# Kernel optimization log

Hardware: AMD Instinct MI355X
Metric: run time of the kernel (lower is better)

Reference implementation:

```python
import jax, jax.numpy as jnp
import numpy as np
from jax import lax

PATCH = 32  # enc conv kernel/stride
EPS = 1e-12  # F.normalize eps


def setup_inputs() -> dict:
    key = jax.random.key(0)
    ks = jax.random.split(key, 7)
    B, N, H, W = 32, 256, 32, 32
    fdim, vdim = 512, 128
    x = jax.random.normal(ks[0], (B, 3 * N, H, W), dtype=jnp.float32)
    conv_w = jax.random.normal(ks[1], (fdim, 3, PATCH, PATCH), dtype=jnp.float32) * (1.0 / np.sqrt(3 * PATCH * PATCH))
    conv_b = jax.random.normal(ks[2], (fdim,), dtype=jnp.float32) * 0.01
    fc1_w = jax.random.normal(ks[3], (vdim, fdim), dtype=jnp.float32) * (1.0 / np.sqrt(fdim))
    fc1_b = jax.random.normal(ks[4], (vdim,), dtype=jnp.float32) * 0.01
    # deterministic dropout masks (p=0.5, train mode -> keep * 1/(1-p))
    drop1 = (jax.random.uniform(ks[5], (B, N, N)) >= 0.5).astype(jnp.float32) * 2.0
    drop2 = (jax.random.uniform(ks[6], (B, N, N)) >= 0.5).astype(jnp.float32) * 2.0
    return {"x": x, "conv_w": conv_w, "conv_b": conv_b,
            "fc1_w": fc1_w, "fc1_b": fc1_b, "drop1": drop1, "drop2": drop2}


def _branch(scores, drop, eye):
    # softmax over dim=-2, zero diag, dropout, L1-normalize over dim=-2
    P = jax.nn.softmax(scores, axis=-2)
    P = P * (1.0 - eye)
    P = P * drop
    denom = jnp.maximum(jnp.sum(jnp.abs(P), axis=-2, keepdims=True), EPS)
    return P / denom


def reference(x, conv_w, conv_b, fc1_w, fc1_b, drop1, drop2):
    B, C, H, W = x.shape
    N = C // 3
    xi = x.reshape(B * N, 3, H, W)
    # enc: patchify conv -> (B*N, fdim, 1, 1)
    fm = lax.conv_general_dilated(xi, conv_w, (PATCH, PATCH), 'VALID',
                                  dimension_numbers=('NCHW', 'OIHW', 'NCHW'))
    fm = fm + conv_b[None, :, None, None]
    # map2vec: adaptive avgpool(1,1) + flatten + fc1
    v = fm.mean(axis=(2, 3))                      # (B*N, fdim)
    v = v @ fc1_w.T + fc1_b                       # (B*N, vdim)
    f = v.reshape(B, N, -1)                       # (B, N, vdim)
    f_norm = f / jnp.maximum(jnp.linalg.norm(f, axis=-1, keepdims=True), EPS)
    A = jnp.einsum('bnd,bmd->bnm', f_norm, f_norm)  # cosine affinity (B,N,N)
    Atemp = A * (128.0 ** 0.5)                    # torch.div(A, 1/128**0.5)
    eye = jnp.eye(N, dtype=A.dtype)
    A1 = _branch(Atemp, drop1, eye)
    A2t = _branch(jnp.swapaxes(Atemp, -1, -2), drop2, eye)
    AtA = jnp.swapaxes(jnp.matmul(A2t, A1), -1, -2)
    # nll_loss(AtA, arange targets) == -mean of diagonal entries
    diag = jnp.einsum('bii->bi', AtA)
    loss = -jnp.mean(diag)
    return f, A, loss
```

## Files before the change

kernel.cpp:

```cpp
#include <hip/hip_runtime.h>
#include <stdint.h>

#define S_SCALE 11.313708498984761f
#define EPS 1e-12f

typedef __bf16 bf16x8 __attribute__((ext_vector_type(8)));
typedef float  f32x4  __attribute__((ext_vector_type(4)));

__device__ __forceinline__ f32x4 mfma16(bf16x8 a, bf16x8 b, f32x4 c) {
  return __builtin_amdgcn_mfma_f32_16x16x32_bf16(a, b, c, 0, 0, 0);
}

__device__ __forceinline__ float waveSum(float v) {
#pragma unroll
  for (int m = 32; m > 0; m >>= 1) v += __shfl_xor(v, m, 64);
  return v;
}

__device__ __forceinline__ void load_lds16(const float* g, float* l) {
  __builtin_amdgcn_global_load_lds(
      (const __attribute__((address_space(1))) uint32_t*)g,
      (__attribute__((address_space(3))) uint32_t*)l, 16, 0, 0);
}

#define OFF_W    0
#define OFF_BIAS 786432
#define OFF_FN   786944
#define OFF_ZP   2884096
#define OFF_P1   3146240

__global__ __launch_bounds__(256) void k_fusew2(const float* __restrict__ conv_w,
                                                const float* __restrict__ fc1_w,
                                                const float* __restrict__ conv_b,
                                                const float* __restrict__ fc1_b,
                                                __bf16* __restrict__ W,
                                                float* __restrict__ bias2,
                                                float* __restrict__ loss) {
  const int t = threadIdx.x;
  const int wave = t >> 6, lane = t & 63;
  if (blockIdx.x == 256) {
    if (t == 0) loss[0] = 0.f;
    for (int o = wave; o < 128; o += 4) {
      float p = 0.f;
#pragma unroll
      for (int c8 = 0; c8 < 8; ++c8)
        p = fmaf(fc1_w[o * 512 + c8 * 64 + lane], conv_b[c8 * 64 + lane], p);
      p = waveSum(p);
      if (lane == 0) bias2[o] = p + fc1_b[o];
    }
    return;
  }
  __shared__ float cw_s[64][12];
  __shared__ float fc1_s[128][65];
  const int k0 = blockIdx.x * 12;
  const int og = t >> 1, half = t & 1;
  const int kb = half * 6;
  float acc[6] = {};
  for (int cs = 0; cs < 8; ++cs) {
    const int cc = cs * 64;
    __syncthreads();
#pragma unroll
    for (int i = 0; i < 3; ++i) {
      int idx = t + 256 * i;
      int cr = idx / 12, kk = idx - cr * 12;
      cw_s[cr][kk] = conv_w[(cc + cr) * 3072 + k0 + kk];
    }
#pragma unroll
    for (int i = 0; i < 2; ++i) {
      int idx = t + 256 * i;
      int o = idx >> 2, c16 = (idx & 3) * 16;
#pragma unroll
      for (int q = 0; q < 4; ++q) {
        float4 v = *(const float4*)&fc1_w[o * 512 + cc + c16 + q * 4];
        fc1_s[o][c16 + q * 4 + 0] = v.x; fc1_s[o][c16 + q * 4 + 1] = v.y;
        fc1_s[o][c16 + q * 4 + 2] = v.z; fc1_s[o][c16 + q * 4 + 3] = v.w;
      }
    }
    __syncthreads();
    for (int ci = 0; ci < 64; ++ci) {
      float fv = fc1_s[og][ci];
#pragma unroll
      for (int j = 0; j < 6; ++j)
        acc[j] = fmaf(fv, cw_s[ci][kb + j], acc[j]);
    }
  }
#pragma unroll
  for (int j = 0; j < 6; ++j)
    W[og * 3072 + k0 + kb + j] = (__bf16)acc[j];
}


#define A_READS(BUF, AV)                                                      \
  _Pragma("unroll") for (int ks = 0; ks < 2; ++ks)                            \
      _Pragma("unroll") for (int mi = 0; mi < 2; ++mi) {                      \
    const int rb = (l15 + mi * 16) * 64;                                      \
    AV[ks][mi][0] =                                                           \
        *(const float4*)&A_lds[BUF][rb + (((ks * 8 + quad * 2) ^ l15) << 2)]; \
    AV[ks][mi][1] =                                                           \
        *(const float4*)&A_lds[BUF][rb + (((ks * 8 + quad * 2 + 1) ^ l15) << 2)]; \
  }

#define PREFETCH(IT, BUF, BB)                                                 \
  {                                                                           \
    const int kn = kbase + (IT) * 64;                                         \
    _Pragma("unroll") for (int j = 0; j < 2; ++j)                             \
        load_lds16(x + (m0 + dr[j]) * 3072 + kn + dc[j],                      \
                   &A_lds[BUF][(wave * 2 + j) * 256]);                        \
    _Pragma("unroll") for (int ks = 0; ks < 2; ++ks)                          \
        _Pragma("unroll") for (int ni = 0; ni < 2; ++ni)                      \
            BB[ks][ni] = *(const uint4*)(bp0 + ni * 49152 + (IT) * 64 + ks * 32); \
  }

#define COMPUTE(AV, BB)                                                       \
  _Pragma("unroll") for (int ks = 0; ks < 2; ++ks) {                          \
    bf16x8 afrag[2];                                                          \
    _Pragma("unroll") for (int mi = 0; mi < 2; ++mi) {                        \
      union { __bf16 h[8]; bf16x8 v; } pk;                                    \
      float4 lo = AV[ks][mi][0], hi = AV[ks][mi][1];                          \
      pk.h[0] = (__bf16)lo.x; pk.h[1] = (__bf16)lo.y;                         \
      pk.h[2] = (__bf16)lo.z; pk.h[3] = (__bf16)lo.w;                         \
      pk.h[4] = (__bf16)hi.x; pk.h[5] = (__bf16)hi.y;                         \
      pk.h[6] = (__bf16)hi.z; pk.h[7] = (__bf16)hi.w;                         \
      afrag[mi] = pk.v;                                                       \
    }                                                                         \
    _Pragma("unroll") for (int mi = 0; mi < 2; ++mi)                          \
        _Pragma("unroll") for (int ni = 0; ni < 2; ++ni)                      \
            acc[mi][ni] =                                                     \
        mfma16(afrag[mi], *(const bf16x8*)&BB[ks][ni], acc[mi][ni]);          \
  }

__global__ __launch_bounds__(256, 8) void k_gemm1(
    const float* __restrict__ x, const __bf16* __restrict__ W,
    float* __restrict__ P0, float* __restrict__ P1, float* __restrict__ P2,
    float* __restrict__ P3, float* __restrict__ P4, float* __restrict__ P5,
    float* __restrict__ P6, float* __restrict__ P7) {
  __shared__ __align__(16) float A_lds[2][32 * 64];
  const int t = threadIdx.x;
  const int wave = t >> 6, lane = t & 63;
  const int l15 = lane & 15, quad = lane >> 4;
  const int m0 = blockIdx.x * 32;
  const int kbase = blockIdx.y * 384;
  float* const Ps[8] = {P0, P1, P2, P3, P4, P5, P6, P7};
  float* P = Ps[blockIdx.y];

  int dr[2], dc[2];
#pragma unroll
  for (int j = 0; j < 2; ++j) {
    int row = wave * 8 + j * 4 + (lane >> 4);
    int cl = (lane & 15) ^ (row & 15);
    dr[j] = row;
    dc[j] = cl * 4;
  }
  const __bf16* bp0 = W + (wave * 32 + l15) * 3072 + quad * 8 + kbase;

  f32x4 acc[2][2] = {{{0.f,0.f,0.f,0.f},{0.f,0.f,0.f,0.f}},
                     {{0.f,0.f,0.f,0.f},{0.f,0.f,0.f,0.f}}};
  uint4 bA[2][2], bB[2][2];
  float4 av[2][2][2];

  PREFETCH(0, 0, bA)
  for (int it2 = 0; it2 < 3; ++it2) {
    const int it = it2 * 2;
    __syncthreads();
    A_READS(0, av)
    if (it + 1 < 6) PREFETCH(it + 1, 1, bB)
    COMPUTE(av, bA)
    __syncthreads();
    A_READS(1, av)
    if (it + 2 < 6) PREFETCH(it + 2, 0, bA)
    COMPUTE(av, bB)
  }
#pragma unroll
  for (int mi = 0; mi < 2; ++mi)
#pragma unroll
    for (int ni = 0; ni < 2; ++ni) {
      int col = wave * 32 + ni * 16 + l15;
#pragma unroll
      for (int r = 0; r < 4; ++r) {
        int row = m0 + mi * 16 + quad * 4 + r;
        P[row * 128 + col] = acc[mi][ni][r];
      }
    }
}

__global__ __launch_bounds__(256) void k_fin(
    float* __restrict__ f_inout, const float* __restrict__ P1,
    const float* __restrict__ P2, const float* __restrict__ P3,
    const float* __restrict__ P4, const float* __restrict__ P5,
    const float* __restrict__ P6, const float* __restrict__ P7,
    const float* __restrict__ bias2, __bf16* __restrict__ fn) {
  const int wave = threadIdx.x >> 6, lane = threadIdx.x & 63;
  const int row = blockIdx.x * 4 + wave;
  const int i0 = row * 128 + lane, i1 = i0 + 64;
  float v0 = f_inout[i0] + P1[i0] + P2[i0] + P3[i0] + P4[i0] + P5[i0] +
             P6[i0] + P7[i0] + bias2[lane];
  float v1 = f_inout[i1] + P1[i1] + P2[i1] + P3[i1] + P4[i1] + P5[i1] +
             P6[i1] + P7[i1] + bias2[lane + 64];
  float ss = waveSum(fmaf(v0, v0, v1 * v1));
  float inv = 1.f / fmaxf(sqrtf(ss), EPS);
  f_inout[i0] = v0;
  f_inout[i1] = v1;
  fn[i0] = (__bf16)(v0 * inv);
  fn[i1] = (__bf16)(v1 * inv);
}

__global__ __launch_bounds__(256) void k_gemm2(const __bf16* __restrict__ fn,
                                               const float* __restrict__ d1,
                                               const float* __restrict__ d2,
                                               float* __restrict__ Aout,
                                               float* __restrict__ Zp) {
  __shared__ __align__(16) __bf16 Li[64][136];
  __shared__ __align__(16) __bf16 Lj[64][136];
  __shared__ float zred[2][4][64];
  const int t = threadIdx.x;
  const int b = blockIdx.y;
  const int ti = blockIdx.x >> 2, tj = blockIdx.x & 3;
  const int i0 = ti * 64, j0 = tj * 64;
  const int wave = t >> 6, lane = t & 63;
  const int l15 = lane & 15, quad = lane >> 4;
  const __bf16* fb = fn + b * 32768;
#pragma unroll
  for (int i = 0; i < 4; ++i) {
    int idx = t + 256 * i;
    int r = idx >> 4, c8 = (idx & 15) * 8;
    *(uint4*)&Li[r][c8] = *(const uint4*)&fb[(i0 + r) * 128 + c8];
    *(uint4*)&Lj[r][c8] = *(const uint4*)&fb[(j0 + r) * 128 + c8];
  }
  __syncthreads();
  f32x4 acc[4] = {{0.f, 0.f, 0.f, 0.f}, {0.f, 0.f, 0.f, 0.f},
                  {0.f, 0.f, 0.f, 0.f}, {0.f, 0.f, 0.f, 0.f}};
#pragma unroll
  for (int ks = 0; ks < 4; ++ks) {
    bf16x8 af = *(const bf16x8*)&Li[wave * 16 + l15][ks * 32 + quad * 8];
#pragma unroll
    for (int nt = 0; nt < 4; ++nt) {
      bf16x8 bf = *(const bf16x8*)&Lj[nt * 16 + l15][ks * 32 + quad * 8];
      acc[nt] = mfma16(af, bf, acc[nt]);
    }
  }
  const int base = b * 65536;
  float* Ab = Aout + base;
  float z1c[4] = {0.f, 0.f, 0.f, 0.f}, z2c[4] = {0.f, 0.f, 0.f, 0.f};
#pragma unroll
  for (int nt = 0; nt < 4; ++nt) {
    int gj = j0 + nt * 16 + l15;
#pragma unroll
    for (int r = 0; r < 4; ++r) {
      int gi = i0 + wave * 16 + quad * 4 + r;
      float a = acc[nt][r];
      Ab[gi * 256 + gj] = a;
      float e = __expf(fmaf(S_SCALE, a, -S_SCALE));
      if (gi != gj) {
        int idx = base + gi * 256 + gj;
        z1c[nt] = fmaf(e, d1[idx], z1c[nt]);
        z2c[nt] = fmaf(e, d2[idx], z2c[nt]);
      }
    }
  }
#pragma unroll
  for (int nt = 0; nt < 4; ++nt) {
    z1c[nt] += __shfl_xor(z1c[nt], 16, 64);
    z1c[nt] += __shfl_xor(z1c[nt], 32, 64);
    z2c[nt] += __shfl_xor(z2c[nt], 16, 64);
    z2c[nt] += __shfl_xor(z2c[nt], 32, 64);
  }
  if (quad == 0) {
#pragma unroll
    for (int nt = 0; nt < 4; ++nt) {
      zred[0][wave][nt * 16 + l15] = z1c[nt];
      zred[1][wave][nt * 16 + l15] = z2c[nt];
    }
  }
  __syncthreads();
  if (t < 128) {
    int z = t >> 6, c = t & 63;
    float s = zred[z][0][c] + zred[z][1][c] + zred[z][2][c] + zred[z][3][c];
    Zp[(z * 4 + ti) * 8192 + b * 256 + j0 + c] = s;
  }
}

__global__ __launch_bounds__(256) void k_loss(const float* __restrict__ Aout,
                                              const float* __restrict__ d1,
                                              const float* __restrict__ d2,
                                              const float* __restrict__ Zp,
                                              float* __restrict__ loss) {
  __shared__ float d1s[64][65];
  __shared__ float z1s[64], z2s[64];
  __shared__ float red[4];
  const int t = threadIdx.x;
  const int b = blockIdx.y;
  const int ic = blockIdx.x >> 2, kc = blockIdx.x & 3;
  const int i0 = ic * 64, k0 = kc * 64;
  const int base = b * 65536;
  if (t < 64) {
    float s = 0.f;
#pragma unroll
    for (int p = 0; p < 4; ++p) s += Zp[p * 8192 + b * 256 + i0 + t];
    z1s[t] = 1.f / fmaxf(s, EPS);
  } else if (t < 128) {
    float s = 0.f;
#pragma unroll
    for (int p = 0; p < 4; ++p) s += Zp[(4 + p) * 8192 + b * 256 + k0 + t - 64];
    z2s[t - 64] = 1.f / fmaxf(s, EPS);
  }
#pragma unroll
  for (int ii = 0; ii < 16; ++ii) {
    int idx = t + 256 * ii;
    int kr = idx >> 6, ci = idx & 63;
    d1s[kr][ci] = d1[base + (k0 + kr) * 256 + i0 + ci];
  }
  __syncthreads();
  const int kl = t & 63, ig = t >> 6;
  float inv2 = z2s[kl];
  float accv = 0.f;
  for (int ii = 0; ii < 16; ++ii) {
    int il = ig * 16 + ii;
    int idx = base + (i0 + il) * 256 + k0 + kl;
    float a = Aout[idx];
    float e = __expf(fmaf(2.f * S_SCALE, a, -2.f * S_SCALE));
    float v = e * d2[idx] * d1s[kl][il] * z1s[il] * inv2;
    if (i0 + il != k0 + kl) accv += v;
  }
  accv = waveSum(accv);
  if ((t & 63) == 0) red[t >> 6] = accv;
  __syncthreads();
  if (t == 0) {
    float tot = red[0] + red[1] + red[2] + red[3];
    atomicAdd(loss, tot * (-1.f / 8192.f));
  }
}

extern "C" void kernel_launch(void* const* d_in, const int* in_sizes, int n_in,
                              void* d_out, int out_size, void* d_ws,
                              size_t ws_size, hipStream_t stream) {
  const float* x = (const float*)d_in[0];
  const float* conv_w = (const float*)d_in[1];
  const float* conv_b = (const float*)d_in[2];
  const float* fc1_w = (const float*)d_in[3];
  const float* fc1_b = (const float*)d_in[4];
  const float* drop1 = (const float*)d_in[5];
  const float* drop2 = (const float*)d_in[6];
  char* ws = (char*)d_ws;
  __bf16* W = (__bf16*)(ws + OFF_W);
  float* bias2 = (float*)(ws + OFF_BIAS);
  __bf16* fn = (__bf16*)(ws + OFF_FN);
  float* Zp = (float*)(ws + OFF_ZP);
  float* P1 = (float*)(ws + OFF_P1);
  float* P2 = P1 + 1048576;
  float* P3 = P2 + 1048576;
  float* P4 = P3 + 1048576;
  float* P5 = P4 + 1048576;
  float* P6 = P5 + 1048576;
  float* P7 = P6 + 1048576;
  float* f = (float*)d_out;
  float* Aout = f + 1048576;
  float* loss = f + 3145728;

  k_fusew2<<<257, 256, 0, stream>>>(conv_w, fc1_w, conv_b, fc1_b, W, bias2, loss);
  k_gemm1<<<dim3(256, 8), 256, 0, stream>>>(x, W, f, P1, P2, P3, P4, P5, P6, P7);
  k_fin<<<2048, 256, 0, stream>>>(f, P1, P2, P3, P4, P5, P6, P7, bias2, fn);
  k_gemm2<<<dim3(16, 32), 256, 0, stream>>>(fn, drop1, drop2, Aout, Zp);
  k_loss<<<dim3(16, 32), 256, 0, stream>>>(Aout, drop1, drop2, Zp, loss);
}
```

Measured before the change: 269.3 us.

## Retile gemm1 to 128x128 blocks with LDS-staged bf16 weights

The patchify GEMM kernel moves from 32x128 tiles with weights read directly from global memory into registers to 128x128 tiles, where both the fp32 activation tile and the bf16 weight tile go into LDS through direct global-to-LDS loads with XOR swizzling. Each wave now computes a 64x64 sub-tile of 4x4 MFMAs, so each weight value is reused across four times as many rows. The double buffering of the old version is dropped in favour of a single buffer with two barriers per k-step. Occupancy falls and the grid shrinks from 2048 to 512 blocks.

```diff
diff --git a/kernel.cpp b/kernel.cpp
--- a/kernel.cpp
+++ b/kernel.cpp
@@ -17,7 +17,7 @@
   return v;
 }
 
-__device__ __forceinline__ void load_lds16(const float* g, float* l) {
+__device__ __forceinline__ void load_lds16(const void* g, void* l) {
   __builtin_amdgcn_global_load_lds(
       (const __attribute__((address_space(1))) uint32_t*)g,
       (__attribute__((address_space(3))) uint32_t*)l, 16, 0, 0);
@@ -89,95 +89,86 @@
     W[og * 3072 + k0 + kb + j] = (__bf16)acc[j];
 }
 
-
-#define A_READS(BUF, AV)                                                      \
-  _Pragma("unroll") for (int ks = 0; ks < 2; ++ks)                            \
-      _Pragma("unroll") for (int mi = 0; mi < 2; ++mi) {                      \
-    const int rb = (l15 + mi * 16) * 64;                                      \
-    AV[ks][mi][0] =                                                           \
-        *(const float4*)&A_lds[BUF][rb + (((ks * 8 + quad * 2) ^ l15) << 2)]; \
-    AV[ks][mi][1] =                                                           \
-        *(const float4*)&A_lds[BUF][rb + (((ks * 8 + quad * 2 + 1) ^ l15) << 2)]; \
-  }
-
-#define PREFETCH(IT, BUF, BB)                                                 \
-  {                                                                           \
-    const int kn = kbase + (IT) * 64;                                         \
-    _Pragma("unroll") for (int j = 0; j < 2; ++j)                             \
-        load_lds16(x + (m0 + dr[j]) * 3072 + kn + dc[j],                      \
-                   &A_lds[BUF][(wave * 2 + j) * 256]);                        \
-    _Pragma("unroll") for (int ks = 0; ks < 2; ++ks)                          \
-        _Pragma("unroll") for (int ni = 0; ni < 2; ++ni)                      \
-            BB[ks][ni] = *(const uint4*)(bp0 + ni * 49152 + (IT) * 64 + ks * 32); \
-  }
-
-#define COMPUTE(AV, BB)                                                       \
-  _Pragma("unroll") for (int ks = 0; ks < 2; ++ks) {                          \
-    bf16x8 afrag[2];                                                          \
-    _Pragma("unroll") for (int mi = 0; mi < 2; ++mi) {                        \
-      union { __bf16 h[8]; bf16x8 v; } pk;                                    \
-      float4 lo = AV[ks][mi][0], hi = AV[ks][mi][1];                          \
-      pk.h[0] = (__bf16)lo.x; pk.h[1] = (__bf16)lo.y;                         \
-      pk.h[2] = (__bf16)lo.z; pk.h[3] = (__bf16)lo.w;                         \
-      pk.h[4] = (__bf16)hi.x; pk.h[5] = (__bf16)hi.y;                         \
-      pk.h[6] = (__bf16)hi.z; pk.h[7] = (__bf16)hi.w;                         \
-      afrag[mi] = pk.v;                                                       \
-    }                                                                         \
-    _Pragma("unroll") for (int mi = 0; mi < 2; ++mi)                          \
-        _Pragma("unroll") for (int ni = 0; ni < 2; ++ni)                      \
-            acc[mi][ni] =                                                     \
-        mfma16(afrag[mi], *(const bf16x8*)&BB[ks][ni], acc[mi][ni]);          \
-  }
-
-__global__ __launch_bounds__(256, 8) void k_gemm1(
+__global__ __launch_bounds__(256, 2) void k_gemm1(
     const float* __restrict__ x, const __bf16* __restrict__ W,
     float* __restrict__ P0, float* __restrict__ P1, float* __restrict__ P2,
     float* __restrict__ P3, float* __restrict__ P4, float* __restrict__ P5,
     float* __restrict__ P6, float* __restrict__ P7) {
-  __shared__ __align__(16) float A_lds[2][32 * 64];
+  __shared__ __align__(16) float As[128 * 64];
+  __shared__ __align__(16) __bf16 Bs[128 * 64];
   const int t = threadIdx.x;
   const int wave = t >> 6, lane = t & 63;
   const int l15 = lane & 15, quad = lane >> 4;
-  const int m0 = blockIdx.x * 32;
+  const int wm = wave >> 1, wn = wave & 1;
+  const int m0 = blockIdx.x * 128;
   const int kbase = blockIdx.y * 384;
   float* const Ps[8] = {P0, P1, P2, P3, P4, P5, P6, P7};
   float* P = Ps[blockIdx.y];
 
-  int dr[2], dc[2];
-#pragma unroll
-  for (int j = 0; j < 2; ++j) {
-    int row = wave * 8 + j * 4 + (lane >> 4);
-    int cl = (lane & 15) ^ (row & 15);
-    dr[j] = row;
-    dc[j] = cl * 4;
-  }
-  const __bf16* bp0 = W + (wave * 32 + l15) * 3072 + quad * 8 + kbase;
-
-  f32x4 acc[2][2] = {{{0.f,0.f,0.f,0.f},{0.f,0.f,0.f,0.f}},
-                     {{0.f,0.f,0.f,0.f},{0.f,0.f,0.f,0.f}}};
-  uint4 bA[2][2], bB[2][2];
-  float4 av[2][2][2];
-
-  PREFETCH(0, 0, bA)
-  for (int it2 = 0; it2 < 3; ++it2) {
-    const int it = it2 * 2;
+  const float* asrc[8];
+  float* adst[8];
+#pragma unroll
+  for (int j = 0; j < 8; ++j) {
+    int r = (wave * 8 + j) * 4 + (lane >> 4);
+    int cl = (lane & 15) ^ (r & 15);
+    asrc[j] = x + (m0 + r) * 3072 + kbase + cl * 4;
+    adst[j] = &As[(wave * 8 + j) * 256];
+  }
+  const __bf16* bsrc[4];
+  __bf16* bdst[4];
+#pragma unroll
+  for (int j = 0; j < 4; ++j) {
+    int r = (wave * 4 + j) * 8 + (lane >> 3);
+    int cl = (lane & 7) ^ (r & 7);
+    bsrc[j] = W + r * 3072 + kbase + cl * 8;
+    bdst[j] = &Bs[(wave * 4 + j) * 512];
+  }
+
+  f32x4 acc[4][4] = {};
+  for (int it = 0; it < 6; ++it) {
     __syncthreads();
-    A_READS(0, av)
-    if (it + 1 < 6) PREFETCH(it + 1, 1, bB)
-    COMPUTE(av, bA)
+#pragma unroll
+    for (int j = 0; j < 8; ++j) load_lds16(asrc[j] + it * 64, adst[j]);
+#pragma unroll
+    for (int j = 0; j < 4; ++j) load_lds16(bsrc[j] + it * 64, bdst[j]);
     __syncthreads();
-    A_READS(1, av)
-    if (it + 2 < 6) PREFETCH(it + 2, 0, bA)
-    COMPUTE(av, bB)
-  }
-#pragma unroll
-  for (int mi = 0; mi < 2; ++mi)
-#pragma unroll
-    for (int ni = 0; ni < 2; ++ni) {
-      int col = wave * 32 + ni * 16 + l15;
+#pragma unroll
+    for (int ks = 0; ks < 2; ++ks) {
+      bf16x8 af[4];
+#pragma unroll
+      for (int mi = 0; mi < 4; ++mi) {
+        int r = wm * 64 + mi * 16 + l15;
+        int rb = r * 64, rx = r & 15;
+        float4 lo = *(const float4*)&As[rb + (((ks * 8 + quad * 2) ^ rx) << 2)];
+        float4 hi = *(const float4*)&As[rb + (((ks * 8 + quad * 2 + 1) ^ rx) << 2)];
+        union { __bf16 h[8]; bf16x8 v; } pk;
+        pk.h[0] = (__bf16)lo.x; pk.h[1] = (__bf16)lo.y;
+        pk.h[2] = (__bf16)lo.z; pk.h[3] = (__bf16)lo.w;
+        pk.h[4] = (__bf16)hi.x; pk.h[5] = (__bf16)hi.y;
+        pk.h[6] = (__bf16)hi.z; pk.h[7] = (__bf16)hi.w;
+        af[mi] = pk.v;
+      }
+      bf16x8 bfr[4];
+#pragma unroll
+      for (int ni = 0; ni < 4; ++ni) {
+        int r = wn * 64 + ni * 16 + l15;
+        bfr[ni] = *(const bf16x8*)&Bs[r * 64 + (((ks * 4 + quad) ^ (r & 7)) << 3)];
+      }
+#pragma unroll
+      for (int mi = 0; mi < 4; ++mi)
+#pragma unroll
+        for (int ni = 0; ni < 4; ++ni)
+          acc[mi][ni] = mfma16(af[mi], bfr[ni], acc[mi][ni]);
+    }
+  }
+#pragma unroll
+  for (int mi = 0; mi < 4; ++mi)
+#pragma unroll
+    for (int ni = 0; ni < 4; ++ni) {
+      int col = wn * 64 + ni * 16 + l15;
 #pragma unroll
       for (int r = 0; r < 4; ++r) {
-        int row = m0 + mi * 16 + quad * 4 + r;
+        int row = m0 + wm * 64 + mi * 16 + quad * 4 + r;
         P[row * 128 + col] = acc[mi][ni][r];
       }
     }
@@ -357,7 +348,7 @@
   float* loss = f + 3145728;
 
   k_fusew2<<<257, 256, 0, stream>>>(conv_w, fc1_w, conv_b, fc1_b, W, bias2, loss);
-  k_gemm1<<<dim3(256, 8), 256, 0, stream>>>(x, W, f, P1, P2, P3, P4, P5, P6, P7);
+  k_gemm1<<<dim3(64, 8), 256, 0, stream>>>(x, W, f, P1, P2, P3, P4, P5, P6, P7);
   k_fin<<<2048, 256, 0, stream>>>(f, P1, P2, P3, P4, P5, P6, P7, bias2, fn);
   k_gemm2<<<dim3(16, 32), 256, 0, stream>>>(fn, drop1, drop2, Aout, Zp);
   k_loss<<<dim3(16, 32), 256, 0, stream>>>(Aout, drop1, drop2, Zp, loss);
```

Measured after the change: 245.2 us. -9.0%, faster.
